# Performance work log

Measured on AMD Instinct MI355X. Metric: run time of the kernel, lower is better.

The kernel has to match this reference:

```python
import jax, jax.numpy as jnp
import numpy as np

SAMPLE_SIZE = 512
DOE_DIM = 10
LATENT = 32
BATCH = 8192
HID = SAMPLE_SIZE // 4   # 128
HID2 = SAMPLE_SIZE // 2  # 256


def _build_groups():
    """Replicates the encoder's per-row neighbor gather construction.
    Returns padded index table [G, Kmax] (int32) and float mask [G, Kmax]."""
    rng = np.random.RandomState(42)
    doe = rng.rand(SAMPLE_SIZE, DOE_DIM)
    sorted_doe = np.argsort(doe, axis=0)  # [S, D]
    idx_list = []
    for i in range(1, SAMPLE_SIZE - 1):
        idxs = np.unique(sorted_doe[i - 1:i + 2, :].flatten())
        idx_list.append(idxs)
    G = len(idx_list)               # sample_size - 2 = 510
    K = max(len(a) for a in idx_list)  # <= 3 * DOE_DIM
    idx = np.zeros((G, K), dtype=np.int32)
    mask = np.zeros((G, K), dtype=np.float32)
    for g, a in enumerate(idx_list):
        idx[g, :len(a)] = a
        mask[g, :len(a)] = 1.0
    return jnp.asarray(idx), jnp.asarray(mask)


def _dense_init(key, fan_in, fan_out):
    w = jax.random.normal(key, (fan_in, fan_out), dtype=jnp.float32) / jnp.sqrt(jnp.float32(fan_in))
    b = jnp.zeros((fan_out,), dtype=jnp.float32)
    return w, b


def setup_inputs() -> dict:
    key = jax.random.key(0)
    ks = jax.random.split(key, 8)
    idx, mask = _build_groups()
    G, K = idx.shape
    x = jax.random.uniform(ks[0], (BATCH, SAMPLE_SIZE), dtype=jnp.float32)
    # per-group Dense(1): weight [G, K] (padded slots zeroed by mask), bias [G]
    gw = jax.random.normal(ks[1], (G, K), dtype=jnp.float32) / jnp.sqrt(jnp.float32(K))
    gb = jnp.zeros((G,), dtype=jnp.float32)
    w1, b1 = _dense_init(ks[2], G, HID)
    w2, b2 = _dense_init(ks[3], HID, LATENT)
    dw1, db1 = _dense_init(ks[4], LATENT, HID)
    dw2, db2 = _dense_init(ks[5], HID, HID2)
    dw3, db3 = _dense_init(ks[6], HID2, SAMPLE_SIZE)
    return {"x": x, "gw": gw, "gb": gb, "w1": w1, "b1": b1, "w2": w2, "b2": b2,
            "dw1": dw1, "db1": db1, "dw2": dw2, "db2": db2, "dw3": dw3, "db3": db3,
            "idx": idx, "mask": mask}


def reference(x, gw, gb, w1, b1, w2, b2, dw1, db1, dw2, db2, dw3, db3, idx, mask):
    # Encoder: grouped gather + per-group Dense(1, relu), fused as one einsum.
    gathered = x[:, idx]                                   # [B, G, K]
    h = jax.nn.relu(jnp.einsum('bgk,gk->bg', gathered, gw * mask) + gb)  # [B, G]
    h = jax.nn.relu(h @ w1 + b1)                           # [B, ss/4]
    z = jax.nn.relu(h @ w2 + b2)                           # [B, latent]
    # Decoder MLP
    d = jax.nn.relu(z @ dw1 + db1)                         # [B, ss/4]
    d = jax.nn.relu(d @ dw2 + db2)                         # [B, ss/2]
    out = jax.nn.sigmoid(d @ dw3 + db3)                    # [B, ss]
    return out
```

## Files before the change

kernel.cpp:

```cpp
#include <hip/hip_runtime.h>
#include <hip/hip_bf16.h>

#define SAMPLE 512
#define GDIM   510
#define HID    128
#define LATENT 32
#define HID2   256
#define TB     32
#define NT     512

typedef unsigned short u16;
typedef unsigned int   u32;
typedef __attribute__((ext_vector_type(8))) short s16x8;
typedef __attribute__((ext_vector_type(4))) float f32x4;

#define WGP_OFF   0
#define W1P_OFF   (WGP_OFF  + 32*16*512)
#define W2P_OFF   (W1P_OFF  + 8*16*512)
#define DW1P_OFF  (W2P_OFF  + 2*4*512)
#define DW2P_OFF  (DW1P_OFF + 8*1*512)
#define DW3P_OFF  (DW2P_OFF + 16*4*512)
#define PACK_U16  (DW3P_OFF + 32*8*512)
#define NCHUNK    (PACK_U16 / 8)
#define NCOPY     8
#define COPY_U16  (1u << 19)
#define NBLK_BW   ((NCHUNK + 255) / 256)

__device__ __forceinline__ u16 f2b(float f) {
    union { float f; u32 i; } v; v.f = f;
    return (u16)((v.i + 0x7FFFu + ((v.i >> 16) & 1u)) >> 16);
}

__global__ __launch_bounds__(256) void build_ws(
    const float* __restrict__ w1, const float* __restrict__ w2,
    const float* __restrict__ dw1, const float* __restrict__ dw2,
    const float* __restrict__ dw3,
    const float* __restrict__ gw, const float* __restrict__ mask,
    const int* __restrict__ idx,
    u16* __restrict__ ws, int G, int K)
{
    int copy = blockIdx.x & 7;
    int c    = (blockIdx.x >> 3) * 256 + threadIdx.x;
    if (c >= NCHUNK) return;
    u16* wsc = ws + (size_t)copy * COPY_U16;
    u16 tmp[8];
    if (c < W1P_OFF / 8) {
        int lane = c & 63;
        int kt   = (c >> 6) & 15;
        int nt   = (c >> 6) >> 4;
        int g    = nt * 16 + (lane & 15);
        int k0   = kt * 32 + (lane >> 4) * 8;
        #pragma unroll
        for (int j = 0; j < 8; ++j) tmp[j] = 0;
        if (g < G) {
            const int*   idxr = idx  + (size_t)g * K;
            const float* gwr  = gw   + (size_t)g * K;
            const float* mr   = mask + (size_t)g * K;
            int t = 0;
            for (; t + 4 <= K; t += 4) {
                int   j0 = idxr[t]     - k0, j1 = idxr[t + 1] - k0;
                int   j2 = idxr[t + 2] - k0, j3 = idxr[t + 3] - k0;
                float m0 = mr[t],     m1 = mr[t + 1];
                float m2 = mr[t + 2], m3 = mr[t + 3];
                float v0 = gwr[t],     v1 = gwr[t + 1];
                float v2 = gwr[t + 2], v3 = gwr[t + 3];
                if ((unsigned)j0 < 8u && m0 > 0.f) tmp[j0] = f2b(v0 * m0);
                if ((unsigned)j1 < 8u && m1 > 0.f) tmp[j1] = f2b(v1 * m1);
                if ((unsigned)j2 < 8u && m2 > 0.f) tmp[j2] = f2b(v2 * m2);
                if ((unsigned)j3 < 8u && m3 > 0.f) tmp[j3] = f2b(v3 * m3);
            }
            for (; t < K; ++t) {
                int j = idxr[t] - k0;
                float m = mr[t];
                if ((unsigned)j < 8u && m > 0.f) tmp[j] = f2b(gwr[t] * m);
            }
        }
        *(s16x8*)(wsc + (size_t)c * 8) = *(s16x8*)tmp;
        return;
    }
    const float* W; int Kd, Nd, KT, base;
    if      (c < W2P_OFF / 8)  { W = w1;  Kd = GDIM;   Nd = HID;    KT = 16; base = W1P_OFF / 8; }
    else if (c < DW1P_OFF / 8) { W = w2;  Kd = HID;    Nd = LATENT; KT = 4;  base = W2P_OFF / 8; }
    else if (c < DW2P_OFF / 8) { W = dw1; Kd = LATENT; Nd = HID;    KT = 1;  base = DW1P_OFF / 8; }
    else if (c < DW3P_OFF / 8) { W = dw2; Kd = HID;    Nd = HID2;   KT = 4;  base = DW2P_OFF / 8; }
    else                       { W = dw3; Kd = HID2;   Nd = SAMPLE; KT = 8;  base = DW3P_OFF / 8; }
    int c2   = c - base;
    int lane = c2 & 63;
    int kt   = (c2 >> 6) % KT;
    int nt   = (c2 >> 6) / KT;
    int n    = nt * 16 + (lane & 15);
    int k0   = kt * 32 + (lane >> 4) * 8;
    #pragma unroll
    for (int j = 0; j < 8; ++j) {
        int k = k0 + j;
        float v = (k < Kd && n < Nd) ? W[(size_t)k * Nd + n] : 0.f;
        tmp[j] = f2b(v);
    }
    *(s16x8*)(wsc + (size_t)c * 8) = *(s16x8*)tmp;
}

template<int KT, int NTN, int TPW>
__device__ __forceinline__ void mfma_phase(
    int wave, int lane,
    const u16* inl, int sin,
    const u16* __restrict__ pW,
    const float* bias,
    u16* outl, int sout)
{
    if (NTN < 8 && wave >= NTN) return;
    const u16* arow0 = inl + (lane & 15) * sin + (lane >> 4) * 8;
    const u16* arow1 = arow0 + 16 * sin;
    f32x4 acc[TPW][2];
    #pragma unroll
    for (int i = 0; i < TPW; ++i) {
        acc[i][0] = (f32x4){0.f, 0.f, 0.f, 0.f};
        acc[i][1] = (f32x4){0.f, 0.f, 0.f, 0.f};
    }
    #pragma unroll
    for (int kt = 0; kt < KT; ++kt) {
        s16x8 a0 = *(const s16x8*)(arow0 + kt * 32);
        s16x8 a1 = *(const s16x8*)(arow1 + kt * 32);
        #pragma unroll
        for (int i = 0; i < TPW; ++i) {
            int nt = wave + 8 * i;
            s16x8 b = *(const s16x8*)(pW + (size_t)((nt * KT + kt) * 64 + lane) * 8);
            acc[i][0] = __builtin_amdgcn_mfma_f32_16x16x32_bf16(a0, b, acc[i][0], 0, 0, 0);
            acc[i][1] = __builtin_amdgcn_mfma_f32_16x16x32_bf16(a1, b, acc[i][1], 0, 0, 0);
        }
    }
    #pragma unroll
    for (int i = 0; i < TPW; ++i) {
        int nt = wave + 8 * i;
        int col = nt * 16 + (lane & 15);
        float bs = bias[col];
        #pragma unroll
        for (int mt = 0; mt < 2; ++mt) {
            #pragma unroll
            for (int r = 0; r < 4; ++r) {
                int row = mt * 16 + (lane >> 4) * 4 + r;
                float v = acc[i][mt][r] + bs;
                outl[row * sout + col] = f2b(v > 0.f ? v : 0.f);
            }
        }
    }
}

#define XS_OFF 0
#define H2_OFF 0
#define ZZ_OFF 4352
#define D1_OFF 5632
#define D2_OFF 9984
#define H1_OFF 18432
#define SMEM_U16 35072

__global__ __launch_bounds__(NT, 2) void ae_mfma(
    const float* __restrict__ x,
    const float* __restrict__ gb,  const float* __restrict__ b1,
    const float* __restrict__ b2,  const float* __restrict__ db1,
    const float* __restrict__ db2, const float* __restrict__ db3,
    const u16*   __restrict__ ws,
    float* __restrict__ out)
{
    __shared__ __align__(16) u16 smem[SMEM_U16];
    __shared__ float biases[1568];
    u16* xs = smem + XS_OFF;
    u16* h1 = smem + H1_OFF;
    u16* h2 = smem + H2_OFF;
    u16* zz = smem + ZZ_OFF;
    u16* d1 = smem + D1_OFF;
    u16* d2 = smem + D2_OFF;

    const int tid  = threadIdx.x;
    const int wave = tid >> 6;
    const int lane = tid & 63;
    const int b0   = blockIdx.x * TB;
    const u16* wsb = ws + (size_t)(blockIdx.x & 7) * COPY_U16;

    biases[tid]        = (tid < GDIM) ? gb[tid] : 0.f;
    biases[1056 + tid] = db3[tid];
    if (tid < 128) biases[512 + tid] = b1[tid];
    if (tid < 32)  biases[640 + tid] = b2[tid];
    if (tid < 128) biases[672 + tid] = db1[tid];
    if (tid < 256) biases[800 + tid] = db2[tid];

    {
        const float4* xg = (const float4*)(x + (size_t)b0 * SAMPLE);
        #pragma unroll
        for (int it = 0; it < (TB * SAMPLE / 4) / NT; ++it) {
            int v = it * NT + tid;
            float4 f = xg[v];
            int row = v >> 7;
            int cp  = (v & 127) * 4;
            u16* p = xs + row * 520 + cp;
            u16 t4[4] = { f2b(f.x), f2b(f.y), f2b(f.z), f2b(f.w) };
            *(unsigned long long*)p = *(unsigned long long*)t4;
        }
    }
    __syncthreads();

    mfma_phase<16, 32, 4>(wave, lane, xs, 520, wsb + WGP_OFF,  biases,       h1, 520);
    __syncthreads();
    mfma_phase<16, 8, 1>(wave, lane, h1, 520, wsb + W1P_OFF,  biases + 512, h2, 136);
    __syncthreads();

    if (wave < 2) {
        const int mt = wave;
        {
            const u16* arow = h2 + (mt * 16 + (lane & 15)) * 136 + (lane >> 4) * 8;
            const u16* pW = wsb + W2P_OFF;
            f32x4 acc[2];
            acc[0] = (f32x4){0.f, 0.f, 0.f, 0.f};
            acc[1] = (f32x4){0.f, 0.f, 0.f, 0.f};
            #pragma unroll
            for (int kt = 0; kt < 4; ++kt) {
                s16x8 a = *(const s16x8*)(arow + kt * 32);
                #pragma unroll
                for (int i = 0; i < 2; ++i) {
                    s16x8 b = *(const s16x8*)(pW + (size_t)((i * 4 + kt) * 64 + lane) * 8);
                    acc[i] = __builtin_amdgcn_mfma_f32_16x16x32_bf16(a, b, acc[i], 0, 0, 0);
                }
            }
            #pragma unroll
            for (int i = 0; i < 2; ++i) {
                int col = i * 16 + (lane & 15);
                float bs = biases[640 + col];
                #pragma unroll
                for (int r = 0; r < 4; ++r) {
                    int row = mt * 16 + (lane >> 4) * 4 + r;
                    float v = acc[i][r] + bs;
                    zz[row * 40 + col] = f2b(v > 0.f ? v : 0.f);
                }
            }
        }
        {
            const u16* arow = zz + (mt * 16 + (lane & 15)) * 40 + (lane >> 4) * 8;
            const u16* pW = wsb + DW1P_OFF;
            s16x8 a = *(const s16x8*)(arow);
            f32x4 acc[8];
            #pragma unroll
            for (int i = 0; i < 8; ++i) {
                s16x8 b = *(const s16x8*)(pW + (size_t)(i * 64 + lane) * 8);
                acc[i] = __builtin_amdgcn_mfma_f32_16x16x32_bf16(
                    a, b, (f32x4){0.f, 0.f, 0.f, 0.f}, 0, 0, 0);
            }
            #pragma unroll
            for (int i = 0; i < 8; ++i) {
                int col = i * 16 + (lane & 15);
                float bs = biases[672 + col];
                #pragma unroll
                for (int r = 0; r < 4; ++r) {
                    int row = mt * 16 + (lane >> 4) * 4 + r;
                    float v = acc[i][r] + bs;
                    d1[row * 136 + col] = f2b(v > 0.f ? v : 0.f);
                }
            }
        }
    }
    __syncthreads();

    mfma_phase<4, 16, 2>(wave, lane, d1, 136, wsb + DW2P_OFF, biases + 800, d2, 264);
    __syncthreads();

    {
        const u16* arow0 = d2 + (lane & 15) * 264 + (lane >> 4) * 8;
        const u16* arow1 = arow0 + 16 * 264;
        const u16* pW = wsb + DW3P_OFF;
        f32x4 acc[4][2];
        #pragma unroll
        for (int i = 0; i < 4; ++i) {
            acc[i][0] = (f32x4){0.f, 0.f, 0.f, 0.f};
            acc[i][1] = (f32x4){0.f, 0.f, 0.f, 0.f};
        }
        #pragma unroll
        for (int kt = 0; kt < 8; ++kt) {
            s16x8 a0 = *(const s16x8*)(arow0 + kt * 32);
            s16x8 a1 = *(const s16x8*)(arow1 + kt * 32);
            #pragma unroll
            for (int i = 0; i < 4; ++i) {
                int nt = wave + 8 * i;
                s16x8 b = *(const s16x8*)(pW + (size_t)((nt * 8 + kt) * 64 + lane) * 8);
                acc[i][0] = __builtin_amdgcn_mfma_f32_16x16x32_bf16(a0, b, acc[i][0], 0, 0, 0);
                acc[i][1] = __builtin_amdgcn_mfma_f32_16x16x32_bf16(a1, b, acc[i][1], 0, 0, 0);
            }
        }
        #pragma unroll
        for (int i = 0; i < 4; ++i) {
            int nt = wave + 8 * i;
            int col = nt * 16 + (lane & 15);
            float bs = biases[1056 + col];
            #pragma unroll
            for (int mt = 0; mt < 2; ++mt) {
                #pragma unroll
                for (int r = 0; r < 4; ++r) {
                    int row = mt * 16 + (lane >> 4) * 4 + r;
                    float v = acc[i][mt][r] + bs;
                    out[(size_t)(b0 + row) * SAMPLE + col] = 1.f / (1.f + __expf(-v));
                }
            }
        }
    }
}

extern "C" void kernel_launch(void* const* d_in, const int* in_sizes, int n_in,
                              void* d_out, int out_size, void* d_ws, size_t ws_size,
                              hipStream_t stream) {
    const float* x   = (const float*)d_in[0];
    const float* gw  = (const float*)d_in[1];
    const float* gb  = (const float*)d_in[2];
    const float* w1  = (const float*)d_in[3];
    const float* b1  = (const float*)d_in[4];
    const float* w2  = (const float*)d_in[5];
    const float* b2  = (const float*)d_in[6];
    const float* dw1 = (const float*)d_in[7];
    const float* db1 = (const float*)d_in[8];
    const float* dw2 = (const float*)d_in[9];
    const float* db2 = (const float*)d_in[10];
    const float* dw3 = (const float*)d_in[11];
    const float* db3 = (const float*)d_in[12];
    const int* idx   = (const int*)d_in[13];
    const float* mask= (const float*)d_in[14];
    float* out = (float*)d_out;
    u16* ws = (u16*)d_ws;

    const int B  = in_sizes[0] / SAMPLE;
    const int G  = in_sizes[2];
    const int K  = in_sizes[1] / G;

    build_ws<<<NCOPY * NBLK_BW, 256, 0, stream>>>(w1, w2, dw1, dw2, dw3,
                                                  gw, mask, idx, ws, G, K);
    ae_mfma<<<B / TB, NT, 0, stream>>>(x, gb, b1, b2, db1, db2, db3, ws, out);
}
```

Baseline: 126.5 us.

## Fuse weight packing into main kernel via cooperative launch and grid sync

Merges the separate weight-packing kernel into the main autoencoder kernel. Each block packs a slice of its copy's bf16 weights, then a grid-wide cooperative sync makes all packed weights visible before the MFMA phases. This removes one kernel launch and its inter-kernel gap, but adds a grid barrier and requires all 256 blocks of 512 threads to be co-resident, which the launch bounds of 2 blocks per CU allow.

```diff
diff --git a/kernel.cpp b/kernel.cpp
--- a/kernel.cpp
+++ b/kernel.cpp
@@ -1,5 +1,6 @@
 #include <hip/hip_runtime.h>
 #include <hip/hip_bf16.h>
+#include <hip/hip_cooperative_groups.h>
 
 #define SAMPLE 512
 #define GDIM   510
@@ -22,27 +23,21 @@
 #define DW3P_OFF  (DW2P_OFF + 16*4*512)
 #define PACK_U16  (DW3P_OFF + 32*8*512)
 #define NCHUNK    (PACK_U16 / 8)
-#define NCOPY     8
 #define COPY_U16  (1u << 19)
-#define NBLK_BW   ((NCHUNK + 255) / 256)
 
 __device__ __forceinline__ u16 f2b(float f) {
     union { float f; u32 i; } v; v.f = f;
     return (u16)((v.i + 0x7FFFu + ((v.i >> 16) & 1u)) >> 16);
 }
 
-__global__ __launch_bounds__(256) void build_ws(
+__device__ __forceinline__ void build_chunk(
+    int c, u16* __restrict__ wsc,
     const float* __restrict__ w1, const float* __restrict__ w2,
     const float* __restrict__ dw1, const float* __restrict__ dw2,
     const float* __restrict__ dw3,
     const float* __restrict__ gw, const float* __restrict__ mask,
-    const int* __restrict__ idx,
-    u16* __restrict__ ws, int G, int K)
+    const int* __restrict__ idx, int G, int K)
 {
-    int copy = blockIdx.x & 7;
-    int c    = (blockIdx.x >> 3) * 256 + threadIdx.x;
-    if (c >= NCHUNK) return;
-    u16* wsc = ws + (size_t)copy * COPY_U16;
     u16 tmp[8];
     if (c < W1P_OFF / 8) {
         int lane = c & 63;
@@ -75,26 +70,25 @@
                 if ((unsigned)j < 8u && m > 0.f) tmp[j] = f2b(gwr[t] * m);
             }
         }
-        *(s16x8*)(wsc + (size_t)c * 8) = *(s16x8*)tmp;
-        return;
-    }
-    const float* W; int Kd, Nd, KT, base;
-    if      (c < W2P_OFF / 8)  { W = w1;  Kd = GDIM;   Nd = HID;    KT = 16; base = W1P_OFF / 8; }
-    else if (c < DW1P_OFF / 8) { W = w2;  Kd = HID;    Nd = LATENT; KT = 4;  base = W2P_OFF / 8; }
-    else if (c < DW2P_OFF / 8) { W = dw1; Kd = LATENT; Nd = HID;    KT = 1;  base = DW1P_OFF / 8; }
-    else if (c < DW3P_OFF / 8) { W = dw2; Kd = HID;    Nd = HID2;   KT = 4;  base = DW2P_OFF / 8; }
-    else                       { W = dw3; Kd = HID2;   Nd = SAMPLE; KT = 8;  base = DW3P_OFF / 8; }
-    int c2   = c - base;
-    int lane = c2 & 63;
-    int kt   = (c2 >> 6) % KT;
-    int nt   = (c2 >> 6) / KT;
-    int n    = nt * 16 + (lane & 15);
-    int k0   = kt * 32 + (lane >> 4) * 8;
-    #pragma unroll
-    for (int j = 0; j < 8; ++j) {
-        int k = k0 + j;
-        float v = (k < Kd && n < Nd) ? W[(size_t)k * Nd + n] : 0.f;
-        tmp[j] = f2b(v);
+    } else {
+        const float* W; int Kd, Nd, KT, base;
+        if      (c < W2P_OFF / 8)  { W = w1;  Kd = GDIM;   Nd = HID;    KT = 16; base = W1P_OFF / 8; }
+        else if (c < DW1P_OFF / 8) { W = w2;  Kd = HID;    Nd = LATENT; KT = 4;  base = W2P_OFF / 8; }
+        else if (c < DW2P_OFF / 8) { W = dw1; Kd = LATENT; Nd = HID;    KT = 1;  base = DW1P_OFF / 8; }
+        else if (c < DW3P_OFF / 8) { W = dw2; Kd = HID;    Nd = HID2;   KT = 4;  base = DW2P_OFF / 8; }
+        else                       { W = dw3; Kd = HID2;   Nd = SAMPLE; KT = 8;  base = DW3P_OFF / 8; }
+        int c2   = c - base;
+        int lane = c2 & 63;
+        int kt   = (c2 >> 6) % KT;
+        int nt   = (c2 >> 6) / KT;
+        int n    = nt * 16 + (lane & 15);
+        int k0   = kt * 32 + (lane >> 4) * 8;
+        #pragma unroll
+        for (int j = 0; j < 8; ++j) {
+            int k = k0 + j;
+            float v = (k < Kd && n < Nd) ? W[(size_t)k * Nd + n] : 0.f;
+            tmp[j] = f2b(v);
+        }
     }
     *(s16x8*)(wsc + (size_t)c * 8) = *(s16x8*)tmp;
 }
@@ -153,13 +147,18 @@
 #define H1_OFF 18432
 #define SMEM_U16 35072
 
-__global__ __launch_bounds__(NT, 2) void ae_mfma(
+__global__ __launch_bounds__(NT, 2) void ae_coop(
     const float* __restrict__ x,
     const float* __restrict__ gb,  const float* __restrict__ b1,
     const float* __restrict__ b2,  const float* __restrict__ db1,
     const float* __restrict__ db2, const float* __restrict__ db3,
-    const u16*   __restrict__ ws,
-    float* __restrict__ out)
+    const float* __restrict__ gw,  const float* __restrict__ mask,
+    const int*   __restrict__ idx,
+    const float* __restrict__ w1,  const float* __restrict__ w2,
+    const float* __restrict__ dw1, const float* __restrict__ dw2,
+    const float* __restrict__ dw3,
+    u16* __restrict__ ws,
+    float* __restrict__ out, int G, int K)
 {
     __shared__ __align__(16) u16 smem[SMEM_U16];
     __shared__ float biases[1568];
@@ -174,7 +173,11 @@
     const int wave = tid >> 6;
     const int lane = tid & 63;
     const int b0   = blockIdx.x * TB;
-    const u16* wsb = ws + (size_t)(blockIdx.x & 7) * COPY_U16;
+    const int copy = blockIdx.x & 7;
+    u16* wsb = ws + (size_t)copy * COPY_U16;
+
+    for (int c = (blockIdx.x >> 3) * NT + tid; c < NCHUNK; c += 32 * NT)
+        build_chunk(c, wsb, w1, w2, dw1, dw2, dw3, gw, mask, idx, G, K);
 
     biases[tid]        = (tid < GDIM) ? gb[tid] : 0.f;
     biases[1056 + tid] = db3[tid];
@@ -182,7 +185,6 @@
     if (tid < 32)  biases[640 + tid] = b2[tid];
     if (tid < 128) biases[672 + tid] = db1[tid];
     if (tid < 256) biases[800 + tid] = db2[tid];
-
     {
         const float4* xg = (const float4*)(x + (size_t)b0 * SAMPLE);
         #pragma unroll
@@ -196,7 +198,8 @@
             *(unsigned long long*)p = *(unsigned long long*)t4;
         }
     }
-    __syncthreads();
+
+    cooperative_groups::this_grid().sync();
 
     mfma_phase<16, 32, 4>(wave, lane, xs, 520, wsb + WGP_OFF,  biases,       h1, 520);
     __syncthreads();
@@ -322,11 +325,16 @@
     float* out = (float*)d_out;
     u16* ws = (u16*)d_ws;
 
-    const int B  = in_sizes[0] / SAMPLE;
-    const int G  = in_sizes[2];
-    const int K  = in_sizes[1] / G;
-
-    build_ws<<<NCOPY * NBLK_BW, 256, 0, stream>>>(w1, w2, dw1, dw2, dw3,
-                                                  gw, mask, idx, ws, G, K);
-    ae_mfma<<<B / TB, NT, 0, stream>>>(x, gb, b1, b2, db1, db2, db3, ws, out);
-}
+    const int B = in_sizes[0] / SAMPLE;
+    int G = in_sizes[2];
+    int K = in_sizes[1] / G;
+
+    void* args[] = {
+        (void*)&x, (void*)&gb, (void*)&b1, (void*)&b2, (void*)&db1,
+        (void*)&db2, (void*)&db3, (void*)&gw, (void*)&mask, (void*)&idx,
+        (void*)&w1, (void*)&w2, (void*)&dw1, (void*)&dw2, (void*)&dw3,
+        (void*)&ws, (void*)&out, (void*)&G, (void*)&K
+    };
+    hipLaunchCooperativeKernel((const void*)ae_coop, dim3(B / TB), dim3(NT),
+                               args, 0, stream);
+}
```

Result: slower. 193.7 us (+53.1%).
